# Performance work log

Hardware: AMD Instinct MI355X
Metric: run time of the kernel (lower is better)

Reference implementation:

```python
import jax, jax.numpy as jnp
import numpy as np
from jax.scipy.linalg import expm

B, HW, SPP, C, H, W = 4, 16384, 3, 64, 128, 128
D_SH = 25
EPS = 1e-8

# color SH mask: higher degrees downweighted (from GaussianAdapter.__init__)
_SH_MASK = np.ones(D_SH, np.float32)
for _d in range(1, 5):
    _SH_MASK[_d * _d:(_d + 1) * (_d + 1)] = 0.1 * 0.25 ** _d

# --- e3nn-style SO(3) generators for wigner_D (precomputed in numpy) ---

def _su2_generators(j):
    m = np.arange(-j, j)
    raising = np.diag(-np.sqrt(j * (j + 1) - m * (m + 1)), k=-1).astype(np.complex128)
    m = np.arange(-j + 1, j + 1)
    lowering = np.diag(np.sqrt(j * (j + 1) - m * (m - 1)), k=1).astype(np.complex128)
    m = np.arange(-j, j + 1)
    return np.stack([0.5 * (raising + lowering), np.diag(1j * m), -0.5j * (raising - lowering)])

def _change_basis(l):
    q = np.zeros((2 * l + 1, 2 * l + 1), dtype=np.complex128)
    for m in range(-l, 0):
        q[l + m, l + abs(m)] = 1 / np.sqrt(2)
        q[l + m, l - abs(m)] = -1j / np.sqrt(2)
    q[l, l] = 1.0
    for m in range(1, l + 1):
        q[l + m, l + abs(m)] = (-1) ** m / np.sqrt(2)
        q[l + m, l - abs(m)] = 1j * (-1) ** m / np.sqrt(2)
    return (-1j) ** l * q

def _so3_generators(l):
    X = _su2_generators(l)
    Q = _change_basis(l)
    return np.real(np.conj(Q.T) @ X @ Q).astype(np.float32)

_SO3 = [_so3_generators(l) for l in range(5)]

# --- small math helpers ---

def _quat_to_mat(q):  # q: (..., 4) wxyz, pytorch3d convention
    r, i, j, k = q[..., 0], q[..., 1], q[..., 2], q[..., 3]
    s = 2.0 / jnp.sum(q * q, axis=-1)
    m = jnp.stack([
        1 - s * (j * j + k * k), s * (i * j - k * r), s * (i * k + j * r),
        s * (i * j + k * r), 1 - s * (i * i + k * k), s * (j * k - i * r),
        s * (i * k - j * r), s * (j * k + i * r), 1 - s * (i * i + j * j)], -1)
    return m.reshape(q.shape[:-1] + (3, 3))

def _rot_y(a):
    c, s = jnp.cos(a), jnp.sin(a)
    z, o = jnp.zeros_like(a), jnp.ones_like(a)
    return jnp.stack([jnp.stack([c, z, s], -1), jnp.stack([z, o, z], -1), jnp.stack([-s, z, c], -1)], -2)

def _rot_x(a):
    c, s = jnp.cos(a), jnp.sin(a)
    z, o = jnp.zeros_like(a), jnp.ones_like(a)
    return jnp.stack([jnp.stack([o, z, z], -1), jnp.stack([z, c, -s], -1), jnp.stack([z, s, c], -1)], -2)

def _matrix_to_angles(R):  # e3nn matrix_to_angles, YXY convention
    x = R[..., :, 1]  # R @ e_y
    x = x / jnp.linalg.norm(x, axis=-1, keepdims=True)
    beta = jnp.arccos(jnp.clip(x[..., 1], -1.0, 1.0))
    alpha = jnp.arctan2(x[..., 0], x[..., 2])
    A = _rot_y(alpha) @ _rot_x(beta)  # angles_to_matrix(alpha, beta, 0)
    Rp = jnp.swapaxes(A, -1, -2) @ R
    gamma = jnp.arctan2(Rp[..., 0, 2], Rp[..., 0, 0])
    return alpha, beta, gamma

def _wigner_D(l, alpha, beta, gamma):  # alpha/beta/gamma: [b]
    X = jnp.asarray(_SO3[l])
    ea = jax.vmap(expm)(alpha[:, None, None] * X[1])
    eb = jax.vmap(expm)(beta[:, None, None] * X[0])
    eg = jax.vmap(expm)(gamma[:, None, None] * X[1])
    return ea @ eb @ eg  # [b, 2l+1, 2l+1]

def _rotate_sh(sh, R):  # sh: [b,hw,spp,3,25], R: [b,3,3]
    alpha, beta, gamma = _matrix_to_angles(R)
    out = []
    for l in range(5):
        D = _wigner_D(l, alpha, -beta, gamma)
        out.append(jnp.einsum('bij,bhscj->bhsci', D, sh[..., l * l:(l + 1) * (l + 1)]))
    return jnp.concatenate(out, axis=-1)

def _forward(extrinsics, intrinsics, coordinates, depths, opacities, raw_gaussians, grd_feat, image_h, image_w):
    scales_raw = raw_gaussians[..., :3]
    rot_raw = raw_gaussians[..., 3:7]
    color_sh = raw_gaussians[..., 7:7 + 3 * D_SH]
    b, c, h, w = grd_feat.shape
    features = jnp.transpose(grd_feat.reshape(b, c, h * w), (0, 2, 1))[:, :, None, :]  # [b,hw,1,c]
    scales = 0.5 + (15.0 - 0.5) * jax.nn.sigmoid(scales_raw)
    pixel_size = jnp.array([1.0 / image_w, 1.0 / image_h], dtype=jnp.float32)
    K2inv = jnp.linalg.inv(intrinsics[..., :2, :2])
    multiplier = 0.1 * jnp.einsum('bij,j->bi', K2inv, pixel_size).sum(-1)  # [b]
    scales = scales * depths[..., None] * multiplier[:, None, None, None]
    rotations = rot_raw / (jnp.linalg.norm(rot_raw, axis=-1, keepdims=True) + EPS)
    color_sh = color_sh.reshape(color_sh.shape[:-1] + (3, D_SH)) * jnp.asarray(_SH_MASK)
    features = jnp.broadcast_to(features, opacities.shape + (c,))
    # covariance = R S S^T R^T
    Rq = _quat_to_mat(rotations)
    covariances = jnp.einsum('...ij,...j,...kj->...ik', Rq, scales * scales, Rq)
    # world rays
    Kinv = jnp.linalg.inv(intrinsics)
    coords_h = jnp.concatenate([coordinates, jnp.ones_like(coordinates[..., :1])], -1)
    dirs = jnp.einsum('bij,bhsj->bhsi', Kinv, coords_h)
    dirs = dirs / jnp.linalg.norm(dirs, axis=-1, keepdims=True)
    Rc2w = extrinsics[..., :3, :3]
    dirs = jnp.einsum('bij,bhsj->bhsi', Rc2w, dirs)
    origins = extrinsics[:, None, None, :3, 3]
    means = origins + dirs * depths[..., None]
    sh_rot = _rotate_sh(color_sh, Rc2w)
    rotations = jnp.broadcast_to(rotations, scales.shape[:-1] + (4,))
    return (means, covariances, sh_rot, opacities, features, scales, rotations)

def setup_inputs() -> dict:
    key = jax.random.key(0)
    ks = jax.random.split(key, 8)
    q = jax.random.normal(ks[0], (B, 4), jnp.float32)
    q = q / jnp.linalg.norm(q, axis=-1, keepdims=True)
    R = _quat_to_mat(q)
    t = jax.random.normal(ks[1], (B, 3), jnp.float32)
    extrinsics = jnp.tile(jnp.eye(4, dtype=jnp.float32), (B, 1, 1)).at[:, :3, :3].set(R).at[:, :3, 3].set(t)
    f = jax.random.uniform(ks[2], (B, 2), jnp.float32, 0.4, 0.6)
    intrinsics = (jnp.zeros((B, 3, 3), jnp.float32)
                  .at[:, 0, 0].set(f[:, 0]).at[:, 1, 1].set(f[:, 1])
                  .at[:, 0, 2].set(0.5).at[:, 1, 2].set(0.5).at[:, 2, 2].set(1.0))
    coordinates = jax.random.uniform(ks[3], (B, HW, SPP, 2), jnp.float32)
    depths = jax.random.uniform(ks[4], (B, HW, SPP), jnp.float32) * 50.0 + 0.5
    opacities = jax.random.uniform(ks[5], (B, HW, SPP), jnp.float32)
    raw_gaussians = jax.random.normal(ks[6], (B, HW, SPP, 3 + 4 + 3 * D_SH), jnp.float32)
    grd_feat = jax.random.normal(ks[7], (B, C, H, W), jnp.float32)
    return {"extrinsics": extrinsics, "intrinsics": intrinsics, "coordinates": coordinates,
            "depths": depths, "opacities": opacities, "raw_gaussians": raw_gaussians,
            "grd_feat": grd_feat, "image_h": H, "image_w": W}

def reference(extrinsics, intrinsics, coordinates, depths, opacities, raw_gaussians, grd_feat, image_h, image_w):
    return _forward(extrinsics, intrinsics, coordinates, depths, opacities, raw_gaussians, grd_feat, image_h, image_w)
```

## Files before the change

### kernel.cpp

```cpp
#include <hip/hip_runtime.h>
#include <math.h>

#define N_TOT   196608
#define HWSPP   49152
#define RGF     82
#define RGS     83
#define NGB     3072
#define NFB     1024

#define OFF_MEANS 0
#define OFF_COV   589824
#define OFF_SH    2359296
#define OFF_OP    17104896
#define OFF_FEAT  17301504
#define OFF_SCL   29884416
#define OFF_ROT   30474240

__device__ __constant__ int c_loff[5] = {0, 1, 10, 35, 84};

__device__ __forceinline__ float sigmoidf_(float x) { return 1.0f / (1.0f + expf(-x)); }

__global__ __launch_bounds__(64) void setup_kernel(
    const float* __restrict__ extr, const float* __restrict__ intr,
    const int* __restrict__ img_h, const int* __restrict__ img_w,
    float* __restrict__ ws)
{
  const int b = blockIdx.x / 5;
  const int l = blockIdx.x % 5;
  const int n = 2 * l + 1;
  const int nn = n * n;
  const int t = threadIdx.x;

  __shared__ double Qr[81], Qi[81], X0c[81], X0r[81], X1r[81];
  __shared__ double E[3][81], A_[81], P_[81], T_[81], M1[81];
  __shared__ double ang[3];
  __shared__ int sS;

  if (t == 0) {
    const float* Ex = extr + b * 16;
    double R00 = Ex[0], R01 = Ex[1], R02 = Ex[2];
    double R11 = Ex[5];
    double R20 = Ex[8], R21 = Ex[9], R22 = Ex[10];
    double x0 = R01, x1 = R11, x2 = R21;
    double nr = sqrt(x0 * x0 + x1 * x1 + x2 * x2);
    x0 /= nr; x1 /= nr; x2 /= nr;
    double beta  = acos(fmin(1.0, fmax(-1.0, x1)));
    double alpha = atan2(x0, x2);
    double ca = cos(alpha), sa = sin(alpha);
    double gamma = atan2(ca * R02 - sa * R22, ca * R00 - sa * R20);
    ang[0] = alpha; ang[1] = beta; ang[2] = gamma;
    if (l == 0) {
      const float* K = intr + b * 9;
      double k00=K[0],k01=K[1],k02=K[2],k10=K[3],k11=K[4],k12=K[5],k20=K[6],k21=K[7],k22=K[8];
      double det = k00*(k11*k22-k12*k21) - k01*(k10*k22-k12*k20) + k02*(k10*k21-k11*k20);
      double id = 1.0 / det;
      float* kv = ws + 660 + b * 9;
      kv[0] = (float)((k11*k22-k12*k21)*id);
      kv[1] = (float)((k02*k21-k01*k22)*id);
      kv[2] = (float)((k01*k12-k02*k11)*id);
      kv[3] = (float)((k12*k20-k10*k22)*id);
      kv[4] = (float)((k00*k22-k02*k20)*id);
      kv[5] = (float)((k02*k10-k00*k12)*id);
      kv[6] = (float)((k10*k21-k11*k20)*id);
      kv[7] = (float)((k01*k20-k00*k21)*id);
      kv[8] = (float)((k00*k11-k01*k10)*id);
      double d2 = k00 * k11 - k01 * k10;
      double ps0 = 1.0 / (double)img_w[0];
      double ps1 = 1.0 / (double)img_h[0];
      double sum = (k11 * ps0 - k01 * ps1 - k10 * ps0 + k00 * ps1) / d2;
      ws[696 + b] = (float)(0.1 * sum);
    }
  }
  for (int e = t; e < 81; e += 64) { Qr[e] = 0.0; Qi[e] = 0.0; X0c[e] = 0.0; }
  __syncthreads();
  if (t == 0) {
    const double irt2 = 0.70710678118654752440;
    for (int m = -l; m < 0; ++m) {
      Qr[(l + m) * n + (l - m)] = irt2;
      Qi[(l + m) * n + (l + m)] = -irt2;
    }
    Qr[l * n + l] = 1.0;
    for (int m = 1; m <= l; ++m) {
      double sg = (m & 1) ? -1.0 : 1.0;
      Qr[(l + m) * n + (l + m)] = sg * irt2;
      Qi[(l + m) * n + (l - m)] = sg * irt2;
    }
    for (int i = 0; i < n - 1; ++i) {
      double mi = (double)(-l + i);
      double ci = sqrt((double)(l * (l + 1)) - mi * (mi + 1.0));
      X0c[i * n + (i + 1)] = 0.5 * ci;
      X0c[(i + 1) * n + i] = -0.5 * ci;
    }
  }
  __syncthreads();
  for (int e = t; e < nn; e += 64) {
    int i = e / n, j = e % n; double s = 0, s2 = 0;
    for (int k = 0; k < n; ++k) { s += X0c[i*n+k]*Qr[k*n+j]; s2 += X0c[i*n+k]*Qi[k*n+j]; }
    A_[e] = s; P_[e] = s2;
  }
  __syncthreads();
  for (int e = t; e < nn; e += 64) {
    int a = e / n, c = e % n; double s = 0, s1 = 0;
    for (int r = 0; r < n; ++r) {
      s  += Qr[r*n+a]*A_[r*n+c] + Qi[r*n+a]*P_[r*n+c];
      double mr = (double)(r - l);
      s1 += mr * (Qi[r*n+a]*Qr[r*n+c] - Qr[r*n+a]*Qi[r*n+c]);
    }
    X0r[e] = s; X1r[e] = s1;
  }
  __syncthreads();

  for (int g = 0; g < 3; ++g) {
    const double* X = (g == 1) ? X0r : X1r;
    double th = (g == 0) ? ang[0] : ((g == 1) ? -ang[1] : ang[2]);
    if (t == 0) {
      double mx = 0.0;
      for (int i = 0; i < n; ++i) {
        double rs = 0.0;
        for (int j = 0; j < n; ++j) rs += fabs(th * X[i * n + j]);
        mx = fmax(mx, rs);
      }
      int s = 0;
      while (mx > 0.25) { mx *= 0.5; ++s; }
      sS = s;
    }
    __syncthreads();
    const int sq = sS;
    double ths = th;
    for (int q = 0; q < sq; ++q) ths *= 0.5;
    for (int e = t; e < nn; e += 64) {
      A_[e] = ths * X[e];
      P_[e] = A_[e];
      E[g][e] = ((e / n) == (e % n) ? 1.0 : 0.0) + A_[e];
    }
    __syncthreads();
    for (int k = 2; k <= 14; ++k) {
      for (int e = t; e < nn; e += 64) {
        int i = e / n, j = e % n; double s = 0;
        for (int kk = 0; kk < n; ++kk) s += P_[i*n+kk] * A_[kk*n+j];
        T_[e] = s;
      }
      __syncthreads();
      for (int e = t; e < nn; e += 64) { P_[e] = T_[e] / (double)k; E[g][e] += P_[e]; }
      __syncthreads();
    }
    for (int q = 0; q < sq; ++q) {
      for (int e = t; e < nn; e += 64) {
        int i = e / n, j = e % n; double s = 0;
        for (int kk = 0; kk < n; ++kk) s += E[g][i*n+kk] * E[g][kk*n+j];
        T_[e] = s;
      }
      __syncthreads();
      for (int e = t; e < nn; e += 64) E[g][e] = T_[e];
      __syncthreads();
    }
  }
  for (int e = t; e < nn; e += 64) {
    int i = e / n, j = e % n; double s = 0;
    for (int k = 0; k < n; ++k) s += E[0][i*n+k] * E[1][k*n+j];
    M1[e] = s;
  }
  __syncthreads();
  for (int e = t; e < nn; e += 64) {
    int i = e / n, j = e % n; double s = 0;
    for (int k = 0; k < n; ++k) s += M1[i*n+k] * E[2][k*n+j];
    ws[b * 165 + c_loff[l] + e] = (float)s;
  }
}

__global__ __launch_bounds__(256) void main_kernel(
    const float* __restrict__ extr,
    const float* __restrict__ coords,
    const float* __restrict__ depths,
    const float* __restrict__ opac,
    const float* __restrict__ rg,
    const float* __restrict__ gf,
    const float* __restrict__ ws,
    float* __restrict__ out)
{
  __shared__ __align__(16) float smem[11584];
  const int t = threadIdx.x;

  if (blockIdx.x >= NGB) {
    float* tile = smem;
    const int blk = blockIdx.x - NGB;
    const int b = blk >> 8;
    const int hw0 = (blk & 255) << 6;
    const int tx = t & 63, ty = t >> 6;
    const float* src = gf + (size_t)b * 64 * 16384 + hw0;
#pragma unroll
    for (int i = 0; i < 16; ++i) {
      int c = i * 4 + ty;
      tile[c * 65 + tx] = src[(size_t)c * 16384 + tx];
    }
    __syncthreads();
    float* dst = out + OFF_FEAT + ((size_t)(b * 16384 + hw0)) * 3 * 64;
    for (int r = ty; r < 192; r += 4) {
      int hw = r / 3;
      dst[(size_t)r * 64 + tx] = tile[tx * 65 + hw];
    }
    return;
  }

  float* sIn    = smem;
  float* sSh    = smem + 5312;
  float* sSmall = smem + 10112;
  float* sD     = smem + 11392;
  float* sKinv  = smem + 11557;
  float* sRc    = smem + 11566;
  float* sOrig  = smem + 11575;
  float* sMult  = smem + 11578;

  const int g0 = blockIdx.x * 64;
  const int b  = g0 / HWSPP;

  if (t < 165) sD[t] = ws[b * 165 + t];
  else if (t < 174) sKinv[t - 165] = ws[660 + b * 9 + (t - 165)];
  else if (t < 183) { int k = t - 174; sRc[k] = extr[b * 16 + (k / 3) * 4 + (k % 3)]; }
  else if (t < 186) sOrig[t - 183] = extr[b * 16 + (t - 183) * 4 + 3];
  else if (t == 186) sMult[0] = ws[696 + b];

  {
    const float4* src4 = (const float4*)(rg + (size_t)g0 * RGF);
    for (int idx = t; idx < (64 * RGF) / 4; idx += 256) {
      float4 v = src4[idx];
      int base = idx * 4;
      int gg = base / RGF;
      int ff = base - gg * RGF;
      float vv[4] = {v.x, v.y, v.z, v.w};
#pragma unroll
      for (int e = 0; e < 4; ++e) {
        int g2 = gg, f2 = ff + e;
        if (f2 >= RGF) { g2 += 1; f2 -= RGF; }
        sIn[g2 * RGS + f2] = vv[e];
      }
    }
  }
  __syncthreads();

  if (t < 64) {
    const int gidx = g0 + t;
    const float* q = &sIn[t * RGS];
    const float dpt = depths[gidx];
    const float mlt = sMult[0];
    float sc0 = (0.5f + 14.5f * sigmoidf_(q[0])) * dpt * mlt;
    float sc1 = (0.5f + 14.5f * sigmoidf_(q[1])) * dpt * mlt;
    float sc2 = (0.5f + 14.5f * sigmoidf_(q[2])) * dpt * mlt;
    float r0 = q[3], r1 = q[4], r2 = q[5], r3 = q[6];
    float nr = sqrtf(r0*r0 + r1*r1 + r2*r2 + r3*r3) + 1e-8f;
    float qr = r0/nr, qi = r1/nr, qj = r2/nr, qk = r3/nr;
    float s2 = 2.0f / (qr*qr + qi*qi + qj*qj + qk*qk);
    float R00 = 1.0f - s2*(qj*qj + qk*qk);
    float R01 = s2*(qi*qj - qk*qr);
    float R02 = s2*(qi*qk + qj*qr);
    float R10 = s2*(qi*qj + qk*qr);
    float R11 = 1.0f - s2*(qi*qi + qk*qk);
    float R12 = s2*(qj*qk - qi*qr);
    float R20 = s2*(qi*qk - qj*qr);
    float R21 = s2*(qj*qk + qi*qr);
    float R22 = 1.0f - s2*(qi*qi + qj*qj);
    float v0 = sc0*sc0, v1 = sc1*sc1, v2 = sc2*sc2;
    float C00 = R00*R00*v0 + R01*R01*v1 + R02*R02*v2;
    float C01 = R00*R10*v0 + R01*R11*v1 + R02*R12*v2;
    float C02 = R00*R20*v0 + R01*R21*v1 + R02*R22*v2;
    float C11 = R10*R10*v0 + R11*R11*v1 + R12*R12*v2;
    float C12 = R10*R20*v0 + R11*R21*v1 + R12*R22*v2;
    float C22 = R20*R20*v0 + R21*R21*v1 + R22*R22*v2;
    float2 cxy = ((const float2*)coords)[gidx];
    float dx = sKinv[0]*cxy.x + sKinv[1]*cxy.y + sKinv[2];
    float dy = sKinv[3]*cxy.x + sKinv[4]*cxy.y + sKinv[5];
    float dz = sKinv[6]*cxy.x + sKinv[7]*cxy.y + sKinv[8];
    float inr = 1.0f / sqrtf(dx*dx + dy*dy + dz*dz);
    dx *= inr; dy *= inr; dz *= inr;
    float wx = sRc[0]*dx + sRc[1]*dy + sRc[2]*dz;
    float wy = sRc[3]*dx + sRc[4]*dy + sRc[5]*dz;
    float wz = sRc[6]*dx + sRc[7]*dy + sRc[8]*dz;
    sSmall[t*3+0] = sOrig[0] + wx * dpt;
    sSmall[t*3+1] = sOrig[1] + wy * dpt;
    sSmall[t*3+2] = sOrig[2] + wz * dpt;
    float* cc = &sSmall[192 + t*9];
    cc[0]=C00; cc[1]=C01; cc[2]=C02; cc[3]=C01; cc[4]=C11; cc[5]=C12; cc[6]=C02; cc[7]=C12; cc[8]=C22;
    float* ss = &sSmall[768 + t*3]; ss[0]=sc0; ss[1]=sc1; ss[2]=sc2;
    float* rr = &sSmall[960 + t*4]; rr[0]=qr; rr[1]=qi; rr[2]=qj; rr[3]=qk;
    sSmall[1216 + t] = opac[gidx];
  } else {
    const int task = t - 64;
    const int gg = task & 63;
    const int ch = task >> 6;
    const float* shin = &sIn[gg * RGS + 7 + ch * 25];
    float* shout = &sSh[gg * 75 + ch * 25];
    float in_[25];
#pragma unroll
    for (int j = 0; j < 25; ++j) in_[j] = shin[j];
    shout[0] = sD[0] * in_[0];
#pragma unroll
    for (int i = 0; i < 3; ++i) {
      float a = sD[1+i*3]*in_[1] + sD[1+i*3+1]*in_[2] + sD[1+i*3+2]*in_[3];
      shout[1 + i] = (float)(0.1 * 0.25) * a;
    }
#pragma unroll
    for (int i = 0; i < 5; ++i) {
      float a = 0.f;
#pragma unroll
      for (int j = 0; j < 5; ++j) a += sD[10 + i*5 + j] * in_[4 + j];
      shout[4 + i] = (float)(0.1 * 0.0625) * a;
    }
#pragma unroll
    for (int i = 0; i < 7; ++i) {
      float a = 0.f;
#pragma unroll
      for (int j = 0; j < 7; ++j) a += sD[35 + i*7 + j] * in_[9 + j];
      shout[9 + i] = (float)(0.1 * 0.015625) * a;
    }
#pragma unroll
    for (int i = 0; i < 9; ++i) {
      float a = 0.f;
#pragma unroll
      for (int j = 0; j < 9; ++j) a += sD[84 + i*9 + j] * in_[16 + j];
      shout[16 + i] = (float)(0.1 * 0.00390625) * a;
    }
  }
  __syncthreads();

  {
    float4* osh = (float4*)(out + OFF_SH + (size_t)g0 * 75);
    const float4* s4 = (const float4*)sSh;
    for (int idx = t; idx < 1200; idx += 256) osh[idx] = s4[idx];
    float* om  = out + OFF_MEANS + (size_t)g0 * 3;
    float* oc  = out + OFF_COV   + (size_t)g0 * 9;
    float* os  = out + OFF_SCL   + (size_t)g0 * 3;
    float* orr = out + OFF_ROT   + (size_t)g0 * 4;
    float* oo  = out + OFF_OP    + (size_t)g0;
    if (t < 192) { om[t] = sSmall[t]; os[t] = sSmall[768 + t]; }
    for (int idx = t; idx < 576; idx += 256) oc[idx] = sSmall[192 + idx];
    orr[t] = sSmall[960 + t];
    if (t < 64) oo[t] = sSmall[1216 + t];
  }
}

extern "C" void kernel_launch(void* const* d_in, const int* in_sizes, int n_in,
                              void* d_out, int out_size, void* d_ws, size_t ws_size,
                              hipStream_t stream)
{
  const float* extr   = (const float*)d_in[0];
  const float* intr   = (const float*)d_in[1];
  const float* coords = (const float*)d_in[2];
  const float* depths = (const float*)d_in[3];
  const float* opac   = (const float*)d_in[4];
  const float* rg     = (const float*)d_in[5];
  const float* gf     = (const float*)d_in[6];
  const int*   ih     = (const int*)d_in[7];
  const int*   iw     = (const int*)d_in[8];
  float* out = (float*)d_out;
  float* ws  = (float*)d_ws;

  hipLaunchKernelGGL(setup_kernel, dim3(20), dim3(64), 0, stream, extr, intr, ih, iw, ws);
  hipLaunchKernelGGL(main_kernel, dim3(NGB + NFB), dim3(256), 0, stream,
                     extr, coords, depths, opac, rg, gf, ws, out);
}
```

Baseline: 287.7 us.

## Replace two matrix exponentials in Wigner-D setup with closed-form z-rotations

The setup kernel builds the Wigner-D matrix for each batch and degree. It now evaluates the alpha and gamma rotation factors analytically, as cos/sin mixing of the m and -m entries, instead of computing two extra matrix exponentials. The single remaining exponential for beta uses a fixed scaling of 2^6 with a Taylor series truncated at 12 terms, replacing the adaptive squaring count. It also keeps the Taylor accumulator in registers and double-buffers the power matrices, which removes extra barriers and copies. The fixed scaling assumes |beta| is bounded so the truncated series stays accurate. Since the setup kernel is tiny next to the main kernel, the effect on total time is probably small.

Result: faster. 243.8 us (-15.3%).

```diff
diff --git a/kernel.cpp b/kernel.cpp
--- a/kernel.cpp
+++ b/kernel.cpp
@@ -31,46 +31,44 @@
   const int nn = n * n;
   const int t = threadIdx.x;
 
-  __shared__ double Qr[81], Qi[81], X0c[81], X0r[81], X1r[81];
-  __shared__ double E[3][81], A_[81], P_[81], T_[81], M1[81];
-  __shared__ double ang[3];
-  __shared__ int sS;
-
-  if (t == 0) {
-    const float* Ex = extr + b * 16;
-    double R00 = Ex[0], R01 = Ex[1], R02 = Ex[2];
-    double R11 = Ex[5];
-    double R20 = Ex[8], R21 = Ex[9], R22 = Ex[10];
-    double x0 = R01, x1 = R11, x2 = R21;
-    double nr = sqrt(x0 * x0 + x1 * x1 + x2 * x2);
-    x0 /= nr; x1 /= nr; x2 /= nr;
-    double beta  = acos(fmin(1.0, fmax(-1.0, x1)));
-    double alpha = atan2(x0, x2);
-    double ca = cos(alpha), sa = sin(alpha);
-    double gamma = atan2(ca * R02 - sa * R22, ca * R00 - sa * R20);
-    ang[0] = alpha; ang[1] = beta; ang[2] = gamma;
-    if (l == 0) {
-      const float* K = intr + b * 9;
-      double k00=K[0],k01=K[1],k02=K[2],k10=K[3],k11=K[4],k12=K[5],k20=K[6],k21=K[7],k22=K[8];
-      double det = k00*(k11*k22-k12*k21) - k01*(k10*k22-k12*k20) + k02*(k10*k21-k11*k20);
-      double id = 1.0 / det;
-      float* kv = ws + 660 + b * 9;
-      kv[0] = (float)((k11*k22-k12*k21)*id);
-      kv[1] = (float)((k02*k21-k01*k22)*id);
-      kv[2] = (float)((k01*k12-k02*k11)*id);
-      kv[3] = (float)((k12*k20-k10*k22)*id);
-      kv[4] = (float)((k00*k22-k02*k20)*id);
-      kv[5] = (float)((k02*k10-k00*k12)*id);
-      kv[6] = (float)((k10*k21-k11*k20)*id);
-      kv[7] = (float)((k01*k20-k00*k21)*id);
-      kv[8] = (float)((k00*k11-k01*k10)*id);
-      double d2 = k00 * k11 - k01 * k10;
-      double ps0 = 1.0 / (double)img_w[0];
-      double ps1 = 1.0 / (double)img_h[0];
-      double sum = (k11 * ps0 - k01 * ps1 - k10 * ps0 + k00 * ps1) / d2;
-      ws[696 + b] = (float)(0.1 * sum);
-    }
-  }
+  __shared__ double Qr[81], Qi[81], X0c[81];
+  __shared__ double X0r[81], U[9];
+  __shared__ double A_[81], P0[81], P1[81], E0[81], E1[81];
+
+  const float* Ex = extr + b * 16;
+  double R00 = Ex[0], R01 = Ex[1], R02 = Ex[2];
+  double R11 = Ex[5];
+  double R20 = Ex[8], R21 = Ex[9], R22 = Ex[10];
+  double x0 = R01, x1 = R11, x2 = R21;
+  double nr = sqrt(x0 * x0 + x1 * x1 + x2 * x2);
+  x0 /= nr; x1 /= nr; x2 /= nr;
+  double beta  = acos(fmin(1.0, fmax(-1.0, x1)));
+  double alpha = atan2(x0, x2);
+  double ca_ = cos(alpha), sa_ = sin(alpha);
+  double gamma = atan2(ca_ * R02 - sa_ * R22, ca_ * R00 - sa_ * R20);
+
+  if (l == 0 && t == 0) {
+    const float* K = intr + b * 9;
+    double k00=K[0],k01=K[1],k02=K[2],k10=K[3],k11=K[4],k12=K[5],k20=K[6],k21=K[7],k22=K[8];
+    double det = k00*(k11*k22-k12*k21) - k01*(k10*k22-k12*k20) + k02*(k10*k21-k11*k20);
+    double id = 1.0 / det;
+    float* kv = ws + 660 + b * 9;
+    kv[0] = (float)((k11*k22-k12*k21)*id);
+    kv[1] = (float)((k02*k21-k01*k22)*id);
+    kv[2] = (float)((k01*k12-k02*k11)*id);
+    kv[3] = (float)((k12*k20-k10*k22)*id);
+    kv[4] = (float)((k00*k22-k02*k20)*id);
+    kv[5] = (float)((k02*k10-k00*k12)*id);
+    kv[6] = (float)((k10*k21-k11*k20)*id);
+    kv[7] = (float)((k01*k20-k00*k21)*id);
+    kv[8] = (float)((k00*k11-k01*k10)*id);
+    double d2 = k00 * k11 - k01 * k10;
+    double ps0 = 1.0 / (double)img_w[0];
+    double ps1 = 1.0 / (double)img_h[0];
+    double sum = (k11 * ps0 - k01 * ps1 - k10 * ps0 + k00 * ps1) / d2;
+    ws[696 + b] = (float)(0.1 * sum);
+  }
+
   for (int e = t; e < 81; e += 64) { Qr[e] = 0.0; Qi[e] = 0.0; X0c[e] = 0.0; }
   __syncthreads();
   if (t == 0) {
@@ -96,75 +94,68 @@
   for (int e = t; e < nn; e += 64) {
     int i = e / n, j = e % n; double s = 0, s2 = 0;
     for (int k = 0; k < n; ++k) { s += X0c[i*n+k]*Qr[k*n+j]; s2 += X0c[i*n+k]*Qi[k*n+j]; }
-    A_[e] = s; P_[e] = s2;
+    P0[e] = s; P1[e] = s2;
   }
   __syncthreads();
   for (int e = t; e < nn; e += 64) {
-    int a = e / n, c = e % n; double s = 0, s1 = 0;
+    int a = e / n, c = e % n; double s = 0;
+    for (int r = 0; r < n; ++r) s += Qr[r*n+a]*P0[r*n+c] + Qi[r*n+a]*P1[r*n+c];
+    X0r[e] = s;
+  }
+  if (t < n) {
+    int i = t, j = 2 * l - i; double s1 = 0;
     for (int r = 0; r < n; ++r) {
-      s  += Qr[r*n+a]*A_[r*n+c] + Qi[r*n+a]*P_[r*n+c];
       double mr = (double)(r - l);
-      s1 += mr * (Qi[r*n+a]*Qr[r*n+c] - Qr[r*n+a]*Qi[r*n+c]);
-    }
-    X0r[e] = s; X1r[e] = s1;
-  }
-  __syncthreads();
-
-  for (int g = 0; g < 3; ++g) {
-    const double* X = (g == 1) ? X0r : X1r;
-    double th = (g == 0) ? ang[0] : ((g == 1) ? -ang[1] : ang[2]);
-    if (t == 0) {
-      double mx = 0.0;
-      for (int i = 0; i < n; ++i) {
-        double rs = 0.0;
-        for (int j = 0; j < n; ++j) rs += fabs(th * X[i * n + j]);
-        mx = fmax(mx, rs);
-      }
-      int s = 0;
-      while (mx > 0.25) { mx *= 0.5; ++s; }
-      sS = s;
+      s1 += mr * (Qi[r*n+i]*Qr[r*n+j] - Qr[r*n+i]*Qi[r*n+j]);
+    }
+    U[i] = s1;
+  }
+  __syncthreads();
+
+  const double ths = -beta / 64.0;
+  for (int e = t; e < nn; e += 64) { A_[e] = ths * X0r[e]; P0[e] = A_[e]; }
+  double Ereg[2];
+  {
+    int ii = 0;
+    for (int e = t; e < nn; e += 64) { Ereg[ii++] = ((e/n)==(e%n) ? 1.0 : 0.0) + ths * X0r[e]; }
+  }
+  __syncthreads();
+  double* Pc = P0; double* Pn = P1;
+  for (int k = 2; k <= 12; ++k) {
+    int ii = 0;
+    for (int e = t; e < nn; e += 64) {
+      int i = e / n, j = e % n; double s = 0;
+      for (int kk = 0; kk < n; ++kk) s += Pc[i*n+kk] * A_[kk*n+j];
+      s /= (double)k;
+      Pn[e] = s; Ereg[ii++] += s;
     }
     __syncthreads();
-    const int sq = sS;
-    double ths = th;
-    for (int q = 0; q < sq; ++q) ths *= 0.5;
+    double* tmp = Pc; Pc = Pn; Pn = tmp;
+  }
+  {
+    int ii = 0;
+    for (int e = t; e < nn; e += 64) E0[e] = Ereg[ii++];
+  }
+  __syncthreads();
+  double* Es = E0; double* Ed = E1;
+  for (int q = 0; q < 6; ++q) {
     for (int e = t; e < nn; e += 64) {
-      A_[e] = ths * X[e];
-      P_[e] = A_[e];
-      E[g][e] = ((e / n) == (e % n) ? 1.0 : 0.0) + A_[e];
+      int i = e / n, j = e % n; double s = 0;
+      for (int kk = 0; kk < n; ++kk) s += Es[i*n+kk] * Es[kk*n+j];
+      Ed[e] = s;
     }
     __syncthreads();
-    for (int k = 2; k <= 14; ++k) {
-      for (int e = t; e < nn; e += 64) {
-        int i = e / n, j = e % n; double s = 0;
-        for (int kk = 0; kk < n; ++kk) s += P_[i*n+kk] * A_[kk*n+j];
-        T_[e] = s;
-      }
-      __syncthreads();
-      for (int e = t; e < nn; e += 64) { P_[e] = T_[e] / (double)k; E[g][e] += P_[e]; }
-      __syncthreads();
-    }
-    for (int q = 0; q < sq; ++q) {
-      for (int e = t; e < nn; e += 64) {
-        int i = e / n, j = e % n; double s = 0;
-        for (int kk = 0; kk < n; ++kk) s += E[g][i*n+kk] * E[g][kk*n+j];
-        T_[e] = s;
-      }
-      __syncthreads();
-      for (int e = t; e < nn; e += 64) E[g][e] = T_[e];
-      __syncthreads();
-    }
-  }
+    double* tmp = Es; Es = Ed; Ed = tmp;
+  }
+
   for (int e = t; e < nn; e += 64) {
-    int i = e / n, j = e % n; double s = 0;
-    for (int k = 0; k < n; ++k) s += E[0][i*n+k] * E[1][k*n+j];
-    M1[e] = s;
-  }
-  __syncthreads();
-  for (int e = t; e < nn; e += 64) {
-    int i = e / n, j = e % n; double s = 0;
-    for (int k = 0; k < n; ++k) s += M1[i*n+k] * E[2][k*n+j];
-    ws[b * 165 + c_loff[l] + e] = (float)s;
+    int i = e / n, j = e % n;
+    int i2 = 2 * l - i, j2 = 2 * l - j;
+    double cai = cos(alpha * U[i]), sai = sin(alpha * U[i]);
+    double cgj = cos(gamma * U[j]), sgj = sin(gamma * U[j]);
+    double w1 = cgj * Es[i *n + j] - sgj * Es[i *n + j2];
+    double w2 = cgj * Es[i2*n + j] - sgj * Es[i2*n + j2];
+    ws[b * 165 + c_loff[l] + e] = (float)(cai * w1 + sai * w2);
   }
 }
 
```
